# Optimization experiments

Hardware: AMD Instinct MI355X
Metric: run time of the kernel (lower is better)

Reference implementation:

```python
import jax, jax.numpy as jnp
import numpy as np


def sobel_kernels_3d(dtype=jnp.float32):
    # Standard 3D Sobel: derivative [-1,0,1] along one axis, smoothing [1,2,1]
    # along the other two. Returns shape (3, 1, 3, 3, 3) in OIDHW layout.
    s = jnp.array([1.0, 2.0, 1.0], dtype=dtype)
    d = jnp.array([-1.0, 0.0, 1.0], dtype=dtype)
    kd = jnp.einsum('i,j,k->ijk', d, s, s)  # d/dD
    kh = jnp.einsum('i,j,k->ijk', s, d, s)  # d/dH
    kw = jnp.einsum('i,j,k->ijk', s, s, d)  # d/dW
    return jnp.stack([kd, kh, kw], axis=0)[:, None]  # (3,1,3,3,3)


def _grad3d(x, kernels):
    # x: (B, C, D, H, W) -> flatten (B*C, 1, D, H, W), conv with padding=1.
    B, C, D, H, W = x.shape
    x_ = x.reshape(B * C, 1, D, H, W)
    return jax.lax.conv_general_dilated(
        x_, kernels.astype(x.dtype),
        window_strides=(1, 1, 1),
        padding=((1, 1), (1, 1), (1, 1)),
        dimension_numbers=('NCDHW', 'OIDHW', 'NCDHW'),
    )  # (B*C, 3, D, H, W)


def setup_inputs() -> dict:
    key = jax.random.key(0)
    k1, k2 = jax.random.split(key)
    shape = (4, 4, 64, 128, 128)
    pred = jax.random.normal(k1, shape, dtype=jnp.float32)
    target = jax.random.normal(k2, shape, dtype=jnp.float32)
    return {"pred": pred, "target": target}


def reference(pred, target):
    kernels = sobel_kernels_3d(pred.dtype)
    grad_pred = _grad3d(pred, kernels)
    grad_target = _grad3d(target, kernels)
    # loss_type == 'l1'
    return jnp.mean(jnp.abs(grad_pred - grad_target))
```

## Files before the change

kernel.cpp:

```cpp
#include <hip/hip_runtime.h>

#define NB 16
#define DD 64
#define HH 128
#define WW 128
#define HW (HH * WW)

constexpr int CD = 4;
constexpr int TH = 8;
constexpr int LZ = CD + 2;
constexpr int LY = TH + 2;
constexpr int PL = LY * WW;
constexpr int NPOS = LZ * LY * (WW / 4);
constexpr float INV_COUNT = 1.0f / 50331648.0f;

__global__ void zero_out_kernel(float* out) {
    if (threadIdx.x == 0 && blockIdx.x == 0) out[0] = 0.0f;
}

__global__ __launch_bounds__(256) void sobel_l1_kernel(
    const float* __restrict__ pred,
    const float* __restrict__ target,
    float* __restrict__ out)
{
    __shared__ float t[LZ * PL];
    __shared__ float wsum[4];

    const int tid = threadIdx.x;
    int b = blockIdx.x;
    const int bh = b & 15; b >>= 4;
    const int bc = b & 15; b >>= 4;
    const int bn = b;

    const int h0 = bh * TH;
    const int d0 = bc * CD;
    const size_t nbase = (size_t)bn * (size_t)(DD * HW);

#pragma unroll
    for (int k = 0; k < 8; ++k) {
        const int i = k * 256 + tid;
        if (i < NPOS) {
            const int q4 = i & 31;
            const int ry = i >> 5;
            const int z  = ry / LY;
            const int y  = ry - z * LY;
            const int gd = d0 - 1 + z;
            const int gh = h0 - 1 + y;
            const bool ok = ((unsigned)gd < DD) && ((unsigned)gh < HH);
            const int gdc = min(max(gd, 0), DD - 1);
            const int ghc = min(max(gh, 0), HH - 1);
            const size_t idx = nbase + (size_t)gdc * HW + (size_t)ghc * WW + 4 * q4;
            const float4 p = *(const float4*)(pred + idx);
            const float4 q = *(const float4*)(target + idx);
            const float m = ok ? 1.0f : 0.0f;
            const float4 v = float4{(p.x - q.x) * m, (p.y - q.y) * m,
                                    (p.z - q.z) * m, (p.w - q.w) * m};
            *(float4*)&t[z * PL + y * WW + 4 * q4] = v;
        }
    }
    __syncthreads();

    const int tc = tid & 31;
    const int lh = tid >> 5;

    auto plane_l = [&](int z, float4& A_, float4& Bh_, float4& Bw_) {
        float4 rs[3], rdw[3];
#pragma unroll
        for (int r = 0; r < 3; ++r) {
            const float4 v = *(const float4*)&t[z * PL + (lh + r) * WW + 4 * tc];
            float lm = __shfl_up(v.w, 1, 32);
            float rp = __shfl_down(v.x, 1, 32);
            if (tc == 0)  lm = 0.f;
            if (tc == 31) rp = 0.f;
            rs[r]  = float4{lm  + 2.f * v.x + v.y,
                            v.x + 2.f * v.y + v.z,
                            v.y + 2.f * v.z + v.w,
                            v.z + 2.f * v.w + rp};
            rdw[r] = float4{v.y - lm, v.z - v.x, v.w - v.y, rp - v.z};
        }
        A_  = float4{rs[0].x + 2.f * rs[1].x + rs[2].x,
                     rs[0].y + 2.f * rs[1].y + rs[2].y,
                     rs[0].z + 2.f * rs[1].z + rs[2].z,
                     rs[0].w + 2.f * rs[1].w + rs[2].w};
        Bh_ = float4{rs[2].x - rs[0].x, rs[2].y - rs[0].y,
                     rs[2].z - rs[0].z, rs[2].w - rs[0].w};
        Bw_ = float4{rdw[0].x + 2.f * rdw[1].x + rdw[2].x,
                     rdw[0].y + 2.f * rdw[1].y + rdw[2].y,
                     rdw[0].z + 2.f * rdw[1].z + rdw[2].z,
                     rdw[0].w + 2.f * rdw[1].w + rdw[2].w};
    };

    float4 rA[3], rBh[3], rBw[3];
    plane_l(0, rA[0], rBh[0], rBw[0]);
    plane_l(1, rA[1], rBh[1], rBw[1]);

    float acc = 0.0f;
#pragma unroll
    for (int ld = 0; ld < CD; ++ld) {
        const int s0 = ld % 3, s1 = (ld + 1) % 3, s2 = (ld + 2) % 3;
        plane_l(ld + 2, rA[s2], rBh[s2], rBw[s2]);

        const float4 a0 = rA[s0],  a2 = rA[s2];
        const float4 b0 = rBh[s0], b1 = rBh[s1], b2 = rBh[s2];
        const float4 c0 = rBw[s0], c1 = rBw[s1], c2 = rBw[s2];
        acc += fabsf(a2.x - a0.x) + fabsf(a2.y - a0.y)
             + fabsf(a2.z - a0.z) + fabsf(a2.w - a0.w);
        acc += fabsf(b0.x + 2.f * b1.x + b2.x) + fabsf(b0.y + 2.f * b1.y + b2.y)
             + fabsf(b0.z + 2.f * b1.z + b2.z) + fabsf(b0.w + 2.f * b1.w + b2.w);
        acc += fabsf(c0.x + 2.f * c1.x + c2.x) + fabsf(c0.y + 2.f * c1.y + c2.y)
             + fabsf(c0.z + 2.f * c1.z + c2.z) + fabsf(c0.w + 2.f * c1.w + c2.w);
    }

#pragma unroll
    for (int off = 32; off > 0; off >>= 1)
        acc += __shfl_down(acc, off, 64);
    const int wave = tid >> 6;
    if ((tid & 63) == 0) wsum[wave] = acc;
    __syncthreads();
    if (tid == 0) {
        const float s = wsum[0] + wsum[1] + wsum[2] + wsum[3];
        atomicAdd(out, s * INV_COUNT);
    }
}

extern "C" void kernel_launch(void* const* d_in, const int* in_sizes, int n_in,
                              void* d_out, int out_size, void* d_ws, size_t ws_size,
                              hipStream_t stream) {
    const float* pred   = (const float*)d_in[0];
    const float* target = (const float*)d_in[1];
    float* out = (float*)d_out;

    zero_out_kernel<<<1, 64, 0, stream>>>(out);

    const int nblocks = NB * (DD / CD) * (HH / TH);
    sobel_l1_kernel<<<nblocks, 256, 0, stream>>>(pred, target, out);
}
```

Baseline: 178.6 us.

## Make blocks persistent over depth tiles with double-buffered register-prefetched LDS

```diff
diff --git a/kernel.cpp b/kernel.cpp
--- a/kernel.cpp
+++ b/kernel.cpp
@@ -12,6 +12,7 @@
 constexpr int LY = TH + 2;
 constexpr int PL = LY * WW;
 constexpr int NPOS = LZ * LY * (WW / 4);
+constexpr int NT = 8;
 constexpr float INV_COUNT = 1.0f / 50331648.0f;
 
 __global__ void zero_out_kernel(float* out) {
@@ -23,92 +24,128 @@
     const float* __restrict__ target,
     float* __restrict__ out)
 {
-    __shared__ float t[LZ * PL];
+    __shared__ float t[2][LZ * PL];
     __shared__ float wsum[4];
 
     const int tid = threadIdx.x;
     int b = blockIdx.x;
-    const int bh = b & 15; b >>= 4;
-    const int bc = b & 15; b >>= 4;
-    const int bn = b;
+    const int bh   = b & 15; b >>= 4;
+    const int half = b & 1;  b >>= 1;
+    const int bn   = b;
 
     const int h0 = bh * TH;
-    const int d0 = bc * CD;
+    const int dbase = half * (NT * CD);
     const size_t nbase = (size_t)bn * (size_t)(DD * HW);
 
+    int  soff[8];
+    int  sz[8];
+    bool sokh[8];
+    bool sval[8];
 #pragma unroll
     for (int k = 0; k < 8; ++k) {
         const int i = k * 256 + tid;
-        if (i < NPOS) {
-            const int q4 = i & 31;
-            const int ry = i >> 5;
-            const int z  = ry / LY;
-            const int y  = ry - z * LY;
-            const int gd = d0 - 1 + z;
-            const int gh = h0 - 1 + y;
-            const bool ok = ((unsigned)gd < DD) && ((unsigned)gh < HH);
+        sval[k] = (i < NPOS);
+        const int ii = sval[k] ? i : 0;
+        const int q4 = ii & 31;
+        const int ry = ii >> 5;
+        const int z  = ry / LY;
+        const int y  = ry - z * LY;
+        const int gh = h0 - 1 + y;
+        sokh[k] = (unsigned)gh < HH;
+        soff[k] = min(max(gh, 0), HH - 1) * WW + 4 * q4;
+        sz[k]   = z;
+    }
+
+    float4 sp[8], sq[8];
+
+    auto load_tile = [&](int tau) {
+        const int d0 = dbase + tau * CD;
+#pragma unroll
+        for (int k = 0; k < 8; ++k) {
+            const int gd  = d0 - 1 + sz[k];
             const int gdc = min(max(gd, 0), DD - 1);
-            const int ghc = min(max(gh, 0), HH - 1);
-            const size_t idx = nbase + (size_t)gdc * HW + (size_t)ghc * WW + 4 * q4;
-            const float4 p = *(const float4*)(pred + idx);
-            const float4 q = *(const float4*)(target + idx);
-            const float m = ok ? 1.0f : 0.0f;
-            const float4 v = float4{(p.x - q.x) * m, (p.y - q.y) * m,
-                                    (p.z - q.z) * m, (p.w - q.w) * m};
-            *(float4*)&t[z * PL + y * WW + 4 * q4] = v;
+            const size_t idx = nbase + (size_t)gdc * HW + soff[k];
+            sp[k] = *(const float4*)(pred + idx);
+            sq[k] = *(const float4*)(target + idx);
         }
-    }
-    __syncthreads();
+    };
+
+    auto store_tile = [&](int tau, float* B) {
+        const int d0 = dbase + tau * CD;
+#pragma unroll
+        for (int k = 0; k < 8; ++k) {
+            if (sval[k]) {
+                const int gd = d0 - 1 + sz[k];
+                const float m = (sokh[k] && (unsigned)gd < DD) ? 1.0f : 0.0f;
+                const int i = k * 256 + tid;
+                const float4 v = float4{(sp[k].x - sq[k].x) * m,
+                                        (sp[k].y - sq[k].y) * m,
+                                        (sp[k].z - sq[k].z) * m,
+                                        (sp[k].w - sq[k].w) * m};
+                *(float4*)&B[4 * i] = v;
+            }
+        }
+    };
 
     const int tc = tid & 31;
     const int lh = tid >> 5;
 
-    auto plane_l = [&](int z, float4& A_, float4& Bh_, float4& Bw_) {
-        float4 rs[3], rdw[3];
+    auto compute_tile = [&](const float* B, float& acc) {
+        auto plane_l = [&](int z, float4& A_, float4& Bh_, float4& Bw_) {
+            float4 rs[3], rdw[3];
 #pragma unroll
-        for (int r = 0; r < 3; ++r) {
-            const float4 v = *(const float4*)&t[z * PL + (lh + r) * WW + 4 * tc];
-            float lm = __shfl_up(v.w, 1, 32);
-            float rp = __shfl_down(v.x, 1, 32);
-            if (tc == 0)  lm = 0.f;
-            if (tc == 31) rp = 0.f;
-            rs[r]  = float4{lm  + 2.f * v.x + v.y,
-                            v.x + 2.f * v.y + v.z,
-                            v.y + 2.f * v.z + v.w,
-                            v.z + 2.f * v.w + rp};
-            rdw[r] = float4{v.y - lm, v.z - v.x, v.w - v.y, rp - v.z};
+            for (int r = 0; r < 3; ++r) {
+                const float4 v = *(const float4*)&B[z * PL + (lh + r) * WW + 4 * tc];
+                float lm = __shfl_up(v.w, 1, 32);
+                float rp = __shfl_down(v.x, 1, 32);
+                if (tc == 0)  lm = 0.f;
+                if (tc == 31) rp = 0.f;
+                rs[r]  = float4{lm  + 2.f * v.x + v.y,
+                                v.x + 2.f * v.y + v.z,
+                                v.y + 2.f * v.z + v.w,
+                                v.z + 2.f * v.w + rp};
+                rdw[r] = float4{v.y - lm, v.z - v.x, v.w - v.y, rp - v.z};
+            }
+            A_  = float4{rs[0].x + 2.f * rs[1].x + rs[2].x,
+                         rs[0].y + 2.f * rs[1].y + rs[2].y,
+                         rs[0].z + 2.f * rs[1].z + rs[2].z,
+                         rs[0].w + 2.f * rs[1].w + rs[2].w};
+            Bh_ = float4{rs[2].x - rs[0].x, rs[2].y - rs[0].y,
+                         rs[2].z - rs[0].z, rs[2].w - rs[0].w};
+            Bw_ = float4{rdw[0].x + 2.f * rdw[1].x + rdw[2].x,
+                         rdw[0].y + 2.f * rdw[1].y + rdw[2].y,
+                         rdw[0].z + 2.f * rdw[1].z + rdw[2].z,
+                         rdw[0].w + 2.f * rdw[1].w + rdw[2].w};
+        };
+
+        float4 rA[3], rBh[3], rBw[3];
+        plane_l(0, rA[0], rBh[0], rBw[0]);
+        plane_l(1, rA[1], rBh[1], rBw[1]);
+#pragma unroll
+        for (int ld = 0; ld < CD; ++ld) {
+            const int s0 = ld % 3, s1 = (ld + 1) % 3, s2 = (ld + 2) % 3;
+            plane_l(ld + 2, rA[s2], rBh[s2], rBw[s2]);
+            const float4 a0 = rA[s0],  a2 = rA[s2];
+            const float4 b0 = rBh[s0], b1 = rBh[s1], b2 = rBh[s2];
+            const float4 c0 = rBw[s0], c1 = rBw[s1], c2 = rBw[s2];
+            acc += fabsf(a2.x - a0.x) + fabsf(a2.y - a0.y)
+                 + fabsf(a2.z - a0.z) + fabsf(a2.w - a0.w);
+            acc += fabsf(b0.x + 2.f * b1.x + b2.x) + fabsf(b0.y + 2.f * b1.y + b2.y)
+                 + fabsf(b0.z + 2.f * b1.z + b2.z) + fabsf(b0.w + 2.f * b1.w + b2.w);
+            acc += fabsf(c0.x + 2.f * c1.x + c2.x) + fabsf(c0.y + 2.f * c1.y + c2.y)
+                 + fabsf(c0.z + 2.f * c1.z + c2.z) + fabsf(c0.w + 2.f * c1.w + c2.w);
         }
-        A_  = float4{rs[0].x + 2.f * rs[1].x + rs[2].x,
-                     rs[0].y + 2.f * rs[1].y + rs[2].y,
-                     rs[0].z + 2.f * rs[1].z + rs[2].z,
-                     rs[0].w + 2.f * rs[1].w + rs[2].w};
-        Bh_ = float4{rs[2].x - rs[0].x, rs[2].y - rs[0].y,
-                     rs[2].z - rs[0].z, rs[2].w - rs[0].w};
-        Bw_ = float4{rdw[0].x + 2.f * rdw[1].x + rdw[2].x,
-                     rdw[0].y + 2.f * rdw[1].y + rdw[2].y,
-                     rdw[0].z + 2.f * rdw[1].z + rdw[2].z,
-                     rdw[0].w + 2.f * rdw[1].w + rdw[2].w};
     };
 
-    float4 rA[3], rBh[3], rBw[3];
-    plane_l(0, rA[0], rBh[0], rBw[0]);
-    plane_l(1, rA[1], rBh[1], rBw[1]);
-
     float acc = 0.0f;
-#pragma unroll
-    for (int ld = 0; ld < CD; ++ld) {
-        const int s0 = ld % 3, s1 = (ld + 1) % 3, s2 = (ld + 2) % 3;
-        plane_l(ld + 2, rA[s2], rBh[s2], rBw[s2]);
-
-        const float4 a0 = rA[s0],  a2 = rA[s2];
-        const float4 b0 = rBh[s0], b1 = rBh[s1], b2 = rBh[s2];
-        const float4 c0 = rBw[s0], c1 = rBw[s1], c2 = rBw[s2];
-        acc += fabsf(a2.x - a0.x) + fabsf(a2.y - a0.y)
-             + fabsf(a2.z - a0.z) + fabsf(a2.w - a0.w);
-        acc += fabsf(b0.x + 2.f * b1.x + b2.x) + fabsf(b0.y + 2.f * b1.y + b2.y)
-             + fabsf(b0.z + 2.f * b1.z + b2.z) + fabsf(b0.w + 2.f * b1.w + b2.w);
-        acc += fabsf(c0.x + 2.f * c1.x + c2.x) + fabsf(c0.y + 2.f * c1.y + c2.y)
-             + fabsf(c0.z + 2.f * c1.z + c2.z) + fabsf(c0.w + 2.f * c1.w + c2.w);
+    load_tile(0);
+    store_tile(0, t[0]);
+    __syncthreads();
+    for (int tau = 0; tau < NT; ++tau) {
+        if (tau + 1 < NT) load_tile(tau + 1);
+        compute_tile(t[tau & 1], acc);
+        if (tau + 1 < NT) store_tile(tau + 1, t[(tau + 1) & 1]);
+        __syncthreads();
     }
 
 #pragma unroll
@@ -132,6 +169,6 @@
 
     zero_out_kernel<<<1, 64, 0, stream>>>(out);
 
-    const int nblocks = NB * (DD / CD) * (HH / TH);
+    const int nblocks = NB * 2 * (HH / TH);
     sobel_l1_kernel<<<nblocks, 256, 0, stream>>>(pred, target, out);
 }
```

After: 152.2 us. 14.8% less time.
